# Kernel tuning notes

Hardware: AMD Instinct MI355X
Metric: run time of the kernel (lower is better)

The kernel has to match this reference:

```python
import jax, jax.numpy as jnp
import numpy as np

N = 50000
E = 800000
IN_C = 128
HID = 8
HEADS = 8
OUT_C = 16
NEG_SLOPE = 0.2


def setup_inputs() -> dict:
    key = jax.random.key(0)
    ks = jax.random.split(key, 10)
    x = jax.random.normal(ks[0], (N, IN_C), dtype=jnp.float32)
    edge_index = jax.random.randint(ks[1], (2, E), 0, N, dtype=jnp.int64)
    # layer 1: GATConv(IN_C, HID, heads=HEADS, concat=True)
    s1 = 1.0 / np.sqrt(IN_C)
    W1 = jax.random.normal(ks[2], (HEADS * HID, IN_C), dtype=jnp.float32) * s1
    att_src1 = jax.random.normal(ks[3], (HEADS, HID), dtype=jnp.float32) * 0.1
    att_dst1 = jax.random.normal(ks[4], (HEADS, HID), dtype=jnp.float32) * 0.1
    b1 = jnp.zeros((HEADS * HID,), dtype=jnp.float32)
    # layer 2: GATConv(HEADS*HID, OUT_C, heads=1, concat=False)
    s2 = 1.0 / np.sqrt(HEADS * HID)
    W2 = jax.random.normal(ks[5], (OUT_C, HEADS * HID), dtype=jnp.float32) * s2
    att_src2 = jax.random.normal(ks[6], (1, OUT_C), dtype=jnp.float32) * 0.1
    att_dst2 = jax.random.normal(ks[7], (1, OUT_C), dtype=jnp.float32) * 0.1
    b2 = jnp.zeros((OUT_C,), dtype=jnp.float32)
    return {"x": x, "edge_index": edge_index, "W1": W1, "att_src1": att_src1,
            "att_dst1": att_dst1, "b1": b1, "W2": W2, "att_src2": att_src2,
            "att_dst2": att_dst2, "b2": b2}


def _gat_conv(x, W, att_src, att_dst, bias, src, dst, concat):
    # x: [N, F_in]; W: [H*C, F_in]; att_*: [H, C]
    H, C = att_src.shape
    h = (x @ W.T).reshape(N, H, C)                       # [N, H, C]
    a_src = jnp.einsum('nhc,hc->nh', h, att_src)          # [N, H]
    a_dst = jnp.einsum('nhc,hc->nh', h, att_dst)          # [N, H]
    e = a_src[src] + a_dst[dst]                           # [Etot, H]
    e = jnp.where(e > 0, e, NEG_SLOPE * e)                # LeakyReLU(0.2)
    # segment softmax over edges grouped by destination node
    m = jax.ops.segment_max(e, dst, num_segments=N)       # [N, H]
    e = jnp.exp(e - m[dst])
    denom = jax.ops.segment_sum(e, dst, num_segments=N)   # [N, H]
    alpha = e / (denom[dst] + 1e-16)                      # [Etot, H]
    msg = alpha[:, :, None] * h[src]                      # [Etot, H, C]
    out = jax.ops.segment_sum(msg, dst, num_segments=N)   # [N, H, C]
    if concat:
        out = out.reshape(N, H * C)
    else:
        out = out.mean(axis=1)
    return out + bias


def reference(x, edge_index, W1, att_src1, att_dst1, b1, W2, att_src2, att_dst2, b2):
    # add self-loops (PyG GATConv default)
    loops = jnp.arange(N, dtype=edge_index.dtype)
    src = jnp.concatenate([edge_index[0], loops])
    dst = jnp.concatenate([edge_index[1], loops])
    h = _gat_conv(x, W1, att_src1, att_dst1, b1, src, dst, concat=True)
    h = jax.nn.elu(h)  # dropout is identity in eval mode
    return _gat_conv(h, W2, att_src2, att_dst2, b2, src, dst, concat=False)
```

## Files before the change

### kernel.cpp

```cpp
#include <hip/hip_runtime.h>
#include <hip/hip_fp16.h>
#include <math.h>

#define NN 50000
#define NE 800000
#define ETOT (NE + NN)
#define INC 128
#define F1 64
#define NH 8
#define OC 16
#define NEG 0.2f
#define BSH 7
#define NBUK 391
#define CHUNK_A 4096
#define NBLK_A ((ETOT + CHUNK_A - 1) / CHUNK_A)
#define G1TILE 64
#define NBLK_G1 ((NN + G1TILE - 1) / G1TILE)
#define XR 136

typedef _Float16 half8 __attribute__((ext_vector_type(8)));
typedef float f32x4 __attribute__((ext_vector_type(4)));

__device__ __forceinline__ float leaky(float x){ return x > 0.f ? x : NEG * x; }

__device__ __forceinline__ void getsd(const int* __restrict__ ei, int e, int& s, int& d){
    if (e < NE){ s = ei[e]; d = ei[NE + e]; }
    else { s = e - NE; d = s; }
}


__global__ __launch_bounds__(256) void zero_gbcnt(int* __restrict__ gbcnt){
    int i = blockIdx.x*256 + threadIdx.x;
    if (i < NBUK) gbcnt[i] = 0;
}

__global__ __launch_bounds__(256) void bucket_hist(const int* __restrict__ ei, int* __restrict__ gbcnt){
    __shared__ int bcnt[NBUK];
    int tid = threadIdx.x;
    for (int j = tid; j < NBUK; j += 256) bcnt[j] = 0;
    __syncthreads();
    int e0 = blockIdx.x * CHUNK_A;
    int e1 = e0 + CHUNK_A; if (e1 > ETOT) e1 = ETOT;
    for (int e = e0 + tid; e < e1; e += 256){
        int d = (e < NE) ? ei[NE + e] : e - NE;
        atomicAdd(&bcnt[d >> BSH], 1);
    }
    __syncthreads();
    for (int j = tid; j < NBUK; j += 256)
        if (bcnt[j]) atomicAdd(&gbcnt[j], bcnt[j]);
}

__global__ __launch_bounds__(512) void bucket_scan(const int* __restrict__ gbcnt,
        int* __restrict__ gboff, int* __restrict__ gbcur){
    __shared__ int s[512];
    int t = threadIdx.x;
    int v = (t < NBUK) ? gbcnt[t] : 0;
    s[t] = v; __syncthreads();
    for (int off = 1; off < 512; off <<= 1){
        int u = (t >= off) ? s[t - off] : 0;
        __syncthreads();
        s[t] += u;
        __syncthreads();
    }
    if (t < NBUK){ int ex = s[t] - v; gboff[t] = ex; gbcur[t] = ex; }
    if (t == 0) gboff[NBUK] = ETOT;
}

__global__ __launch_bounds__(256) void bucket_scatter(const int* __restrict__ ei,
        int* __restrict__ gbcur, unsigned* __restrict__ packed){
    __shared__ int bcnt[NBUK];
    int tid = threadIdx.x;
    for (int j = tid; j < NBUK; j += 256) bcnt[j] = 0;
    __syncthreads();
    int e0 = blockIdx.x * CHUNK_A;
    int e1 = e0 + CHUNK_A; if (e1 > ETOT) e1 = ETOT;
    for (int e = e0 + tid; e < e1; e += 256){
        int d = (e < NE) ? ei[NE + e] : e - NE;
        atomicAdd(&bcnt[d >> BSH], 1);
    }
    __syncthreads();
    for (int j = tid; j < NBUK; j += 256){
        int c = bcnt[j];
        bcnt[j] = c ? atomicAdd(&gbcur[j], c) : 0;
    }
    __syncthreads();
    for (int e = e0 + tid; e < e1; e += 256){
        int s, d; getsd(ei, e, s, d);
        int pos = atomicAdd(&bcnt[d >> BSH], 1);
        packed[pos] = ((unsigned)s << 16) | (unsigned)d;
    }
}

__global__ __launch_bounds__(256) void bucket_finalize(const unsigned* __restrict__ packed,
        const int* __restrict__ gboff, int* __restrict__ rowstart, int* __restrict__ esrc){
    __shared__ int ldeg[1 << BSH];
    __shared__ int lcur[1 << BSH];
    __shared__ int wtot[2];
    int b = blockIdx.x, t = threadIdx.x;
    if (t < (1 << BSH)) ldeg[t] = 0;
    __syncthreads();
    int p0 = gboff[b], p1 = gboff[b+1];
    for (int i = p0 + t; i < p1; i += 256)
        atomicAdd(&ldeg[packed[i] & ((1 << BSH) - 1)], 1);
    __syncthreads();
    if (t < (1 << BSH)){
        int v = ldeg[t];
        int lane = t & 63, w = t >> 6;
        int iv = v;
        #pragma unroll
        for (int off = 1; off < 64; off <<= 1){
            int u = __shfl_up(iv, off);
            if (lane >= off) iv += u;
        }
        lcur[t] = iv;
        if (lane == 63) wtot[w] = iv;
    }
    __syncthreads();
    if (t < (1 << BSH)){
        int v = ldeg[t];
        int w = t >> 6;
        int incl = lcur[t] + (w ? wtot[0] : 0);
        int rs = p0 + incl - v;
        int n = (b << BSH) + t;
        if (n < NN) rowstart[n] = rs;
        lcur[t] = rs;
    }
    if (b == 0 && t == 0) rowstart[NN] = ETOT;
    __syncthreads();
    for (int i = p0 + t; i < p1; i += 256){
        unsigned p = packed[i];
        int pos = atomicAdd(&lcur[p & ((1 << BSH) - 1)], 1);
        esrc[pos] = (int)(p >> 16);
    }
}

__global__ __launch_bounds__(256) void gemm1(const float* __restrict__ x, const float* __restrict__ W1,
        const float* __restrict__ att_s, const float* __restrict__ att_d,
        __half* __restrict__ h1h, float* __restrict__ a_src, float* __restrict__ a_dst){
    __shared__ _Float16 xs[64*XR];
    __shared__ _Float16 wsl[64*XR];
    int tid = threadIdx.x;
    int base = blockIdx.x * G1TILE;
    for (int i = tid; i < F1*INC; i += 256){
        int o = i >> 7, k = i & 127;
        wsl[o*XR + k] = (_Float16)W1[i];
    }
    for (int f = tid; f < 64*32; f += 256){
        int row = f >> 5, c4 = f & 31;
        int n = base + row;
        float4 v = (n < NN) ? reinterpret_cast<const float4*>(x)[n*32 + c4]
                            : make_float4(0.f,0.f,0.f,0.f);
        _Float16* p = &xs[row*XR + c4*4];
        p[0] = (_Float16)v.x; p[1] = (_Float16)v.y;
        p[2] = (_Float16)v.z; p[3] = (_Float16)v.w;
    }
    __syncthreads();
    int w = tid >> 6, lane = tid & 63;
    int mrow = lane & 15, kg = lane >> 4;
    int nodeb = w*16;
    half8 afrag[4];
    #pragma unroll
    for (int kk = 0; kk < 4; ++kk){
        const _Float16* pa = &xs[(nodeb + mrow)*XR + kk*32 + kg*4];
        *(unsigned long long*)&afrag[kk]       = *(const unsigned long long*)pa;
        *((unsigned long long*)&afrag[kk] + 1) = *(const unsigned long long*)(pa + 16);
    }
    f32x4 acc[4];
    #pragma unroll
    for (int ot = 0; ot < 4; ++ot) acc[ot] = (f32x4){0.f,0.f,0.f,0.f};
    #pragma unroll
    for (int ot = 0; ot < 4; ++ot){
        #pragma unroll
        for (int kk = 0; kk < 4; ++kk){
            const _Float16* pb = &wsl[(ot*16 + mrow)*XR + kk*32 + kg*4];
            half8 bfrag;
            *(unsigned long long*)&bfrag       = *(const unsigned long long*)pb;
            *((unsigned long long*)&bfrag + 1) = *(const unsigned long long*)(pb + 16);
            acc[ot] = __builtin_amdgcn_mfma_f32_16x16x32_f16(afrag[kk], bfrag, acc[ot], 0, 0, 0);
        }
    }
    #pragma unroll
    for (int ot = 0; ot < 4; ++ot){
        int o = ot*16 + mrow;
        float as_o = att_s[o], ad_o = att_d[o];
        #pragma unroll
        for (int r = 0; r < 4; ++r){
            float dv = acc[ot][r];
            int node = base + nodeb + kg*4 + r;
            if (node < NN) h1h[node*64 + o] = __float2half(dv);
            float ps = dv * as_o, pd = dv * ad_o;
            ps += __shfl_xor(ps, 1); ps += __shfl_xor(ps, 2); ps += __shfl_xor(ps, 4);
            pd += __shfl_xor(pd, 1); pd += __shfl_xor(pd, 2); pd += __shfl_xor(pd, 4);
            if ((lane & 7) == 0 && node < NN){
                int h = ot*2 + ((lane >> 3) & 1);
                a_src[node*8 + h] = ps;
                a_dst[node*8 + h] = pd;
            }
        }
    }
}


__global__ __launch_bounds__(256, 4) void gemm2(const float* __restrict__ out1, const float* __restrict__ W2,
        const float* __restrict__ att_s, const float* __restrict__ att_d,
        __half* __restrict__ h2h, float* __restrict__ a_src, float* __restrict__ a_dst){
    __shared__ float xs2[64*80];
    int tid = threadIdx.x;
    int base = blockIdx.x * 64;
    int w = tid >> 6, lane = tid & 63;
    int o = lane >> 2, ks = lane & 3;
    float4 wr[4];
    {
        const float4* W4 = reinterpret_cast<const float4*>(W2);
        #pragma unroll
        for (int j4 = 0; j4 < 4; ++j4)
            wr[j4] = W4[o*16 + ks*4 + j4];
    }
    float as_o = att_s[o], ad_o = att_d[o];
    {
        #pragma unroll
        for (int j = 0; j < 4; ++j){
            int f = tid + 256*j;
            int row = f >> 4, c4 = f & 15;
            int n = base + row;
            float4 v = make_float4(0.f,0.f,0.f,0.f);
            if (n < NN) v = reinterpret_cast<const float4*>(out1)[n*16 + c4];
            v.x = v.x > 0.f ? v.x : __expf(v.x) - 1.f;
            v.y = v.y > 0.f ? v.y : __expf(v.y) - 1.f;
            v.z = v.z > 0.f ? v.z : __expf(v.z) - 1.f;
            v.w = v.w > 0.f ? v.w : __expf(v.w) - 1.f;
            int sk = c4 >> 2, j4 = c4 & 3;
            *(float4*)(&xs2[row*80 + sk*20 + j4*4]) = v;
        }
    }
    __syncthreads();
    for (int r = 0; r < 16; ++r){
        int row = w*16 + r;
        const float* xb = &xs2[row*80 + ks*20];
        float acc = 0.f;
        #pragma unroll
        for (int j4 = 0; j4 < 4; ++j4){
            float4 xv = *(const float4*)(xb + j4*4);
            acc = fmaf(xv.x, wr[j4].x, acc);
            acc = fmaf(xv.y, wr[j4].y, acc);
            acc = fmaf(xv.z, wr[j4].z, acc);
            acc = fmaf(xv.w, wr[j4].w, acc);
        }
        acc += __shfl_xor(acc, 1); acc += __shfl_xor(acc, 2);
        int node = base + row;
        float ps = acc * as_o, pd = acc * ad_o;
        ps += __shfl_xor(ps, 4); ps += __shfl_xor(ps, 8);
        ps += __shfl_xor(ps, 16); ps += __shfl_xor(ps, 32);
        pd += __shfl_xor(pd, 4); pd += __shfl_xor(pd, 8);
        pd += __shfl_xor(pd, 16); pd += __shfl_xor(pd, 32);
        if (node < NN){
            if (ks == 0) h2h[node*16 + o] = __float2half(acc);
            if (lane == 0){ a_src[node] = ps; a_dst[node] = pd; }
        }
    }
}


__global__ __launch_bounds__(256) void layer1_node(const int* __restrict__ rowstart,
        const int* __restrict__ esrc, const float* __restrict__ a_src,
        const float* __restrict__ a_dst, const __half* __restrict__ h1h,
        const float* __restrict__ b1, float* __restrict__ out1){
    int wid = __builtin_amdgcn_readfirstlane((blockIdx.x*256 + threadIdx.x) >> 6);
    int lane = threadIdx.x & 63;
    if (wid >= NN) return;
    int n = wid;
    int h = lane >> 3;
    int r0 = rowstart[n], r1 = rowstart[n+1];
    float ad = a_dst[n*8 + h];
    float den0 = 0.f, acc0 = 0.f, den1 = 0.f, acc1 = 0.f;
    float den2 = 0.f, acc2 = 0.f, den3 = 0.f, acc3 = 0.f;
    float den4 = 0.f, acc4 = 0.f, den5 = 0.f, acc5 = 0.f;
    float den6 = 0.f, acc6 = 0.f, den7 = 0.f, acc7 = 0.f;
    int i = r0;
    for (; i + 7 < r1; i += 8){
        int s0 = esrc[i],   s1 = esrc[i+1], s2 = esrc[i+2], s3 = esrc[i+3];
        int s4 = esrc[i+4], s5 = esrc[i+5], s6 = esrc[i+6], s7 = esrc[i+7];
        float e0 = leaky(a_src[s0*8 + h] + ad);
        float e1 = leaky(a_src[s1*8 + h] + ad);
        float e2 = leaky(a_src[s2*8 + h] + ad);
        float e3 = leaky(a_src[s3*8 + h] + ad);
        float e4 = leaky(a_src[s4*8 + h] + ad);
        float e5 = leaky(a_src[s5*8 + h] + ad);
        float e6 = leaky(a_src[s6*8 + h] + ad);
        float e7 = leaky(a_src[s7*8 + h] + ad);
        float hv0 = __half2float(h1h[s0*64 + lane]);
        float hv1 = __half2float(h1h[s1*64 + lane]);
        float hv2 = __half2float(h1h[s2*64 + lane]);
        float hv3 = __half2float(h1h[s3*64 + lane]);
        float hv4 = __half2float(h1h[s4*64 + lane]);
        float hv5 = __half2float(h1h[s5*64 + lane]);
        float hv6 = __half2float(h1h[s6*64 + lane]);
        float hv7 = __half2float(h1h[s7*64 + lane]);
        float p0 = __expf(e0), p1 = __expf(e1), p2 = __expf(e2), p3 = __expf(e3);
        float p4 = __expf(e4), p5 = __expf(e5), p6 = __expf(e6), p7 = __expf(e7);
        den0 += p0; acc0 = fmaf(p0, hv0, acc0);
        den1 += p1; acc1 = fmaf(p1, hv1, acc1);
        den2 += p2; acc2 = fmaf(p2, hv2, acc2);
        den3 += p3; acc3 = fmaf(p3, hv3, acc3);
        den4 += p4; acc4 = fmaf(p4, hv4, acc4);
        den5 += p5; acc5 = fmaf(p5, hv5, acc5);
        den6 += p6; acc6 = fmaf(p6, hv6, acc6);
        den7 += p7; acc7 = fmaf(p7, hv7, acc7);
    }
    for (; i + 3 < r1; i += 4){
        int s0 = esrc[i], s1 = esrc[i+1], s2 = esrc[i+2], s3 = esrc[i+3];
        float e0 = leaky(a_src[s0*8 + h] + ad);
        float e1 = leaky(a_src[s1*8 + h] + ad);
        float e2 = leaky(a_src[s2*8 + h] + ad);
        float e3 = leaky(a_src[s3*8 + h] + ad);
        float hv0 = __half2float(h1h[s0*64 + lane]);
        float hv1 = __half2float(h1h[s1*64 + lane]);
        float hv2 = __half2float(h1h[s2*64 + lane]);
        float hv3 = __half2float(h1h[s3*64 + lane]);
        float p0 = __expf(e0), p1 = __expf(e1), p2 = __expf(e2), p3 = __expf(e3);
        den0 += p0; acc0 = fmaf(p0, hv0, acc0);
        den1 += p1; acc1 = fmaf(p1, hv1, acc1);
        den2 += p2; acc2 = fmaf(p2, hv2, acc2);
        den3 += p3; acc3 = fmaf(p3, hv3, acc3);
    }
    for (; i < r1; ++i){
        int s = esrc[i];
        float p = __expf(leaky(a_src[s*8 + h] + ad));
        den0 += p; acc0 = fmaf(p, __half2float(h1h[s*64 + lane]), acc0);
    }
    float den = ((den0 + den1) + (den2 + den3)) + ((den4 + den5) + (den6 + den7));
    float acc = ((acc0 + acc1) + (acc2 + acc3)) + ((acc4 + acc5) + (acc6 + acc7));
    out1[n*64 + lane] = acc/(den + 1e-16f) + b1[lane];
}

__global__ __launch_bounds__(256) void layer2_node(const int* __restrict__ rowstart,
        const int* __restrict__ esrc, const float* __restrict__ a_src,
        const float* __restrict__ a_dst, const __half* __restrict__ h2h,
        const float* __restrict__ b2, float* __restrict__ out){
    int wid = __builtin_amdgcn_readfirstlane((blockIdx.x*256 + threadIdx.x) >> 6);
    int lane = threadIdx.x & 63;
    if (wid >= NN) return;
    int n = wid;
    int slot = lane >> 4, c = lane & 15;
    int r0 = rowstart[n], r1 = rowstart[n+1];
    float ad = a_dst[n];
    float den0 = 0.f, acc0 = 0.f, den1 = 0.f, acc1 = 0.f;
    float den2 = 0.f, acc2 = 0.f, den3 = 0.f, acc3 = 0.f;
    int i = r0 + slot;
    for (; i + 12 < r1; i += 16){
        int s0 = esrc[i], s1 = esrc[i+4], s2 = esrc[i+8], s3 = esrc[i+12];
        float p0 = __expf(leaky(a_src[s0] + ad));
        float p1 = __expf(leaky(a_src[s1] + ad));
        float p2 = __expf(leaky(a_src[s2] + ad));
        float p3 = __expf(leaky(a_src[s3] + ad));
        float hv0 = __half2float(h2h[s0*16 + c]);
        float hv1 = __half2float(h2h[s1*16 + c]);
        float hv2 = __half2float(h2h[s2*16 + c]);
        float hv3 = __half2float(h2h[s3*16 + c]);
        den0 += p0; acc0 = fmaf(p0, hv0, acc0);
        den1 += p1; acc1 = fmaf(p1, hv1, acc1);
        den2 += p2; acc2 = fmaf(p2, hv2, acc2);
        den3 += p3; acc3 = fmaf(p3, hv3, acc3);
    }
    for (; i < r1; i += 4){
        int s = esrc[i];
        float p = __expf(leaky(a_src[s] + ad));
        den0 += p; acc0 = fmaf(p, __half2float(h2h[s*16 + c]), acc0);
    }
    float den = (den0 + den1) + (den2 + den3);
    float acc = (acc0 + acc1) + (acc2 + acc3);
    den += __shfl_xor(den, 16); den += __shfl_xor(den, 32);
    acc += __shfl_xor(acc, 16); acc += __shfl_xor(acc, 32);
    if (slot == 0) out[n*16 + c] = acc/(den + 1e-16f) + b2[c];
}

extern "C" void kernel_launch(void* const* d_in, const int* in_sizes, int n_in,
                              void* d_out, int out_size, void* d_ws, size_t ws_size,
                              hipStream_t stream){
    const float* x    = (const float*)d_in[0];
    const int*   ei   = (const int*)d_in[1];
    const float* W1   = (const float*)d_in[2];
    const float* as1w = (const float*)d_in[3];
    const float* ad1w = (const float*)d_in[4];
    const float* b1   = (const float*)d_in[5];
    const float* W2   = (const float*)d_in[6];
    const float* as2w = (const float*)d_in[7];
    const float* ad2w = (const float*)d_in[8];
    const float* b2   = (const float*)d_in[9];
    float* out = (float*)d_out;

    float* ws = (float*)d_ws;
    __half* h1h     = (__half*)ws;
    float* out1     = ws + (size_t)32*NN;
    int*   rowstart = (int*)(ws + (size_t)96*NN);
    int*   gbcnt    = rowstart + NN + 1;
    int*   gboff    = gbcnt + NBUK;
    int*   gbcur    = gboff + NBUK + 1;
    unsigned* packed= (unsigned*)(gbcur + NBUK);
    int*   esrc     = (int*)(packed + ETOT);
    float* a_src1 = out;
    float* a_dst1 = out + (size_t)8*NN;
    __half* h2h   = h1h;
    float* a_src2 = ws + (size_t)8*NN;
    float* a_dst2 = a_src2 + NN;

    hipLaunchKernelGGL(zero_gbcnt,      dim3(2), dim3(256), 0, stream, gbcnt);
    hipLaunchKernelGGL(bucket_hist,     dim3(NBLK_A), dim3(256), 0, stream, ei, gbcnt);
    hipLaunchKernelGGL(bucket_scan,     dim3(1), dim3(512), 0, stream, gbcnt, gboff, gbcur);
    hipLaunchKernelGGL(bucket_scatter,  dim3(NBLK_A), dim3(256), 0, stream, ei, gbcur, packed);
    hipLaunchKernelGGL(bucket_finalize, dim3(NBUK), dim3(256), 0, stream, packed, gboff, rowstart, esrc);

    hipLaunchKernelGGL(gemm1, dim3(NBLK_G1), dim3(256), 0, stream, x, W1, as1w, ad1w, h1h, a_src1, a_dst1);
    hipLaunchKernelGGL(layer1_node, dim3((NN*64 + 255)/256), dim3(256), 0, stream,
                       rowstart, esrc, a_src1, a_dst1, h1h, b1, out1);
    hipLaunchKernelGGL(gemm2, dim3((NN + 63)/64), dim3(256), 0, stream, out1, W2, as2w, ad2w, h2h, a_src2, a_dst2);
    hipLaunchKernelGGL(layer2_node, dim3((NN*64 + 255)/256), dim3(256), 0, stream,
                       rowstart, esrc, a_src2, a_dst2, h2h, b2, out);
}
```

Baseline: 123.8 us.

## Fuse edge bucket scatter with gemm1 and software-pipeline layer1 gathers

Merges the bucket_scatter and gemm1 kernels into one launch. The first NBLK_A blocks do the edge scatter and the remaining blocks do the feature GEMM, so the two independent stages run side by side and one launch is removed. Separately, the layer1 aggregation loop is restructured to issue the next batch of 8 gathers before computing on the previous batch, so memory latency overlaps with the exp/FMA work. The cost is higher register pressure in layer1_node, and the fused kernel's blocks all carry the gemm shared-memory footprint, which may limit occupancy for the scatter blocks.

```diff
diff --git a/kernel.cpp b/kernel.cpp
--- a/kernel.cpp
+++ b/kernel.cpp
@@ -66,81 +66,38 @@
     if (t == 0) gboff[NBUK] = ETOT;
 }
 
-__global__ __launch_bounds__(256) void bucket_scatter(const int* __restrict__ ei,
-        int* __restrict__ gbcur, unsigned* __restrict__ packed){
-    __shared__ int bcnt[NBUK];
-    int tid = threadIdx.x;
-    for (int j = tid; j < NBUK; j += 256) bcnt[j] = 0;
-    __syncthreads();
-    int e0 = blockIdx.x * CHUNK_A;
-    int e1 = e0 + CHUNK_A; if (e1 > ETOT) e1 = ETOT;
-    for (int e = e0 + tid; e < e1; e += 256){
-        int d = (e < NE) ? ei[NE + e] : e - NE;
-        atomicAdd(&bcnt[d >> BSH], 1);
-    }
-    __syncthreads();
-    for (int j = tid; j < NBUK; j += 256){
-        int c = bcnt[j];
-        bcnt[j] = c ? atomicAdd(&gbcur[j], c) : 0;
-    }
-    __syncthreads();
-    for (int e = e0 + tid; e < e1; e += 256){
-        int s, d; getsd(ei, e, s, d);
-        int pos = atomicAdd(&bcnt[d >> BSH], 1);
-        packed[pos] = ((unsigned)s << 16) | (unsigned)d;
-    }
-}
-
-__global__ __launch_bounds__(256) void bucket_finalize(const unsigned* __restrict__ packed,
-        const int* __restrict__ gboff, int* __restrict__ rowstart, int* __restrict__ esrc){
-    __shared__ int ldeg[1 << BSH];
-    __shared__ int lcur[1 << BSH];
-    __shared__ int wtot[2];
-    int b = blockIdx.x, t = threadIdx.x;
-    if (t < (1 << BSH)) ldeg[t] = 0;
-    __syncthreads();
-    int p0 = gboff[b], p1 = gboff[b+1];
-    for (int i = p0 + t; i < p1; i += 256)
-        atomicAdd(&ldeg[packed[i] & ((1 << BSH) - 1)], 1);
-    __syncthreads();
-    if (t < (1 << BSH)){
-        int v = ldeg[t];
-        int lane = t & 63, w = t >> 6;
-        int iv = v;
-        #pragma unroll
-        for (int off = 1; off < 64; off <<= 1){
-            int u = __shfl_up(iv, off);
-            if (lane >= off) iv += u;
-        }
-        lcur[t] = iv;
-        if (lane == 63) wtot[w] = iv;
-    }
-    __syncthreads();
-    if (t < (1 << BSH)){
-        int v = ldeg[t];
-        int w = t >> 6;
-        int incl = lcur[t] + (w ? wtot[0] : 0);
-        int rs = p0 + incl - v;
-        int n = (b << BSH) + t;
-        if (n < NN) rowstart[n] = rs;
-        lcur[t] = rs;
-    }
-    if (b == 0 && t == 0) rowstart[NN] = ETOT;
-    __syncthreads();
-    for (int i = p0 + t; i < p1; i += 256){
-        unsigned p = packed[i];
-        int pos = atomicAdd(&lcur[p & ((1 << BSH) - 1)], 1);
-        esrc[pos] = (int)(p >> 16);
-    }
-}
-
-__global__ __launch_bounds__(256) void gemm1(const float* __restrict__ x, const float* __restrict__ W1,
+__global__ __launch_bounds__(256) void scatter_gemm1(const int* __restrict__ ei,
+        int* __restrict__ gbcur, unsigned* __restrict__ packed,
+        const float* __restrict__ x, const float* __restrict__ W1,
         const float* __restrict__ att_s, const float* __restrict__ att_d,
         __half* __restrict__ h1h, float* __restrict__ a_src, float* __restrict__ a_dst){
     __shared__ _Float16 xs[64*XR];
     __shared__ _Float16 wsl[64*XR];
     int tid = threadIdx.x;
-    int base = blockIdx.x * G1TILE;
+    if (blockIdx.x < NBLK_A){
+        int* bcnt = (int*)xs;
+        for (int j = tid; j < NBUK; j += 256) bcnt[j] = 0;
+        __syncthreads();
+        int e0 = blockIdx.x * CHUNK_A;
+        int e1 = e0 + CHUNK_A; if (e1 > ETOT) e1 = ETOT;
+        for (int e = e0 + tid; e < e1; e += 256){
+            int d = (e < NE) ? ei[NE + e] : e - NE;
+            atomicAdd(&bcnt[d >> BSH], 1);
+        }
+        __syncthreads();
+        for (int j = tid; j < NBUK; j += 256){
+            int c = bcnt[j];
+            bcnt[j] = c ? atomicAdd(&gbcur[j], c) : 0;
+        }
+        __syncthreads();
+        for (int e = e0 + tid; e < e1; e += 256){
+            int s, d; getsd(ei, e, s, d);
+            int pos = atomicAdd(&bcnt[d >> BSH], 1);
+            packed[pos] = ((unsigned)s << 16) | (unsigned)d;
+        }
+        return;
+    }
+    int base = (blockIdx.x - NBLK_A) * G1TILE;
     for (int i = tid; i < F1*INC; i += 256){
         int o = i >> 7, k = i & 127;
         wsl[o*XR + k] = (_Float16)W1[i];
@@ -197,6 +154,49 @@
                 a_dst[node*8 + h] = pd;
             }
         }
+    }
+}
+
+__global__ __launch_bounds__(256) void bucket_finalize(const unsigned* __restrict__ packed,
+        const int* __restrict__ gboff, int* __restrict__ rowstart, int* __restrict__ esrc){
+    __shared__ int ldeg[1 << BSH];
+    __shared__ int lcur[1 << BSH];
+    __shared__ int wtot[2];
+    int b = blockIdx.x, t = threadIdx.x;
+    if (t < (1 << BSH)) ldeg[t] = 0;
+    __syncthreads();
+    int p0 = gboff[b], p1 = gboff[b+1];
+    for (int i = p0 + t; i < p1; i += 256)
+        atomicAdd(&ldeg[packed[i] & ((1 << BSH) - 1)], 1);
+    __syncthreads();
+    if (t < (1 << BSH)){
+        int v = ldeg[t];
+        int lane = t & 63, w = t >> 6;
+        int iv = v;
+        #pragma unroll
+        for (int off = 1; off < 64; off <<= 1){
+            int u = __shfl_up(iv, off);
+            if (lane >= off) iv += u;
+        }
+        lcur[t] = iv;
+        if (lane == 63) wtot[w] = iv;
+    }
+    __syncthreads();
+    if (t < (1 << BSH)){
+        int v = ldeg[t];
+        int w = t >> 6;
+        int incl = lcur[t] + (w ? wtot[0] : 0);
+        int rs = p0 + incl - v;
+        int n = (b << BSH) + t;
+        if (n < NN) rowstart[n] = rs;
+        lcur[t] = rs;
+    }
+    if (b == 0 && t == 0) rowstart[NN] = ETOT;
+    __syncthreads();
+    for (int i = p0 + t; i < p1; i += 256){
+        unsigned p = packed[i];
+        int pos = atomicAdd(&lcur[p & ((1 << BSH) - 1)], 1);
+        esrc[pos] = (int)(p >> 16);
     }
 }
 
@@ -277,35 +277,68 @@
     float den4 = 0.f, acc4 = 0.f, den5 = 0.f, acc5 = 0.f;
     float den6 = 0.f, acc6 = 0.f, den7 = 0.f, acc7 = 0.f;
     int i = r0;
-    for (; i + 7 < r1; i += 8){
+    int nfull = (r1 - r0) >> 3;
+    if (nfull > 0){
         int s0 = esrc[i],   s1 = esrc[i+1], s2 = esrc[i+2], s3 = esrc[i+3];
         int s4 = esrc[i+4], s5 = esrc[i+5], s6 = esrc[i+6], s7 = esrc[i+7];
-        float e0 = leaky(a_src[s0*8 + h] + ad);
-        float e1 = leaky(a_src[s1*8 + h] + ad);
-        float e2 = leaky(a_src[s2*8 + h] + ad);
-        float e3 = leaky(a_src[s3*8 + h] + ad);
-        float e4 = leaky(a_src[s4*8 + h] + ad);
-        float e5 = leaky(a_src[s5*8 + h] + ad);
-        float e6 = leaky(a_src[s6*8 + h] + ad);
-        float e7 = leaky(a_src[s7*8 + h] + ad);
-        float hv0 = __half2float(h1h[s0*64 + lane]);
-        float hv1 = __half2float(h1h[s1*64 + lane]);
-        float hv2 = __half2float(h1h[s2*64 + lane]);
-        float hv3 = __half2float(h1h[s3*64 + lane]);
-        float hv4 = __half2float(h1h[s4*64 + lane]);
-        float hv5 = __half2float(h1h[s5*64 + lane]);
-        float hv6 = __half2float(h1h[s6*64 + lane]);
-        float hv7 = __half2float(h1h[s7*64 + lane]);
-        float p0 = __expf(e0), p1 = __expf(e1), p2 = __expf(e2), p3 = __expf(e3);
-        float p4 = __expf(e4), p5 = __expf(e5), p6 = __expf(e6), p7 = __expf(e7);
-        den0 += p0; acc0 = fmaf(p0, hv0, acc0);
-        den1 += p1; acc1 = fmaf(p1, hv1, acc1);
-        den2 += p2; acc2 = fmaf(p2, hv2, acc2);
-        den3 += p3; acc3 = fmaf(p3, hv3, acc3);
-        den4 += p4; acc4 = fmaf(p4, hv4, acc4);
-        den5 += p5; acc5 = fmaf(p5, hv5, acc5);
-        den6 += p6; acc6 = fmaf(p6, hv6, acc6);
-        den7 += p7; acc7 = fmaf(p7, hv7, acc7);
+        float eA0 = a_src[s0*8 + h], eA1 = a_src[s1*8 + h];
+        float eA2 = a_src[s2*8 + h], eA3 = a_src[s3*8 + h];
+        float eA4 = a_src[s4*8 + h], eA5 = a_src[s5*8 + h];
+        float eA6 = a_src[s6*8 + h], eA7 = a_src[s7*8 + h];
+        float hA0 = __half2float(h1h[s0*64 + lane]);
+        float hA1 = __half2float(h1h[s1*64 + lane]);
+        float hA2 = __half2float(h1h[s2*64 + lane]);
+        float hA3 = __half2float(h1h[s3*64 + lane]);
+        float hA4 = __half2float(h1h[s4*64 + lane]);
+        float hA5 = __half2float(h1h[s5*64 + lane]);
+        float hA6 = __half2float(h1h[s6*64 + lane]);
+        float hA7 = __half2float(h1h[s7*64 + lane]);
+        i += 8;
+        for (int b = 1; b < nfull; ++b){
+            int t0 = esrc[i],   t1 = esrc[i+1], t2 = esrc[i+2], t3 = esrc[i+3];
+            int t4 = esrc[i+4], t5 = esrc[i+5], t6 = esrc[i+6], t7 = esrc[i+7];
+            float eB0 = a_src[t0*8 + h], eB1 = a_src[t1*8 + h];
+            float eB2 = a_src[t2*8 + h], eB3 = a_src[t3*8 + h];
+            float eB4 = a_src[t4*8 + h], eB5 = a_src[t5*8 + h];
+            float eB6 = a_src[t6*8 + h], eB7 = a_src[t7*8 + h];
+            float hB0 = __half2float(h1h[t0*64 + lane]);
+            float hB1 = __half2float(h1h[t1*64 + lane]);
+            float hB2 = __half2float(h1h[t2*64 + lane]);
+            float hB3 = __half2float(h1h[t3*64 + lane]);
+            float hB4 = __half2float(h1h[t4*64 + lane]);
+            float hB5 = __half2float(h1h[t5*64 + lane]);
+            float hB6 = __half2float(h1h[t6*64 + lane]);
+            float hB7 = __half2float(h1h[t7*64 + lane]);
+            i += 8;
+            float p0 = __expf(leaky(eA0 + ad)), p1 = __expf(leaky(eA1 + ad));
+            float p2 = __expf(leaky(eA2 + ad)), p3 = __expf(leaky(eA3 + ad));
+            float p4 = __expf(leaky(eA4 + ad)), p5 = __expf(leaky(eA5 + ad));
+            float p6 = __expf(leaky(eA6 + ad)), p7 = __expf(leaky(eA7 + ad));
+            den0 += p0; acc0 = fmaf(p0, hA0, acc0);
+            den1 += p1; acc1 = fmaf(p1, hA1, acc1);
+            den2 += p2; acc2 = fmaf(p2, hA2, acc2);
+            den3 += p3; acc3 = fmaf(p3, hA3, acc3);
+            den4 += p4; acc4 = fmaf(p4, hA4, acc4);
+            den5 += p5; acc5 = fmaf(p5, hA5, acc5);
+            den6 += p6; acc6 = fmaf(p6, hA6, acc6);
+            den7 += p7; acc7 = fmaf(p7, hA7, acc7);
+            eA0 = eB0; eA1 = eB1; eA2 = eB2; eA3 = eB3;
+            eA4 = eB4; eA5 = eB5; eA6 = eB6; eA7 = eB7;
+            hA0 = hB0; hA1 = hB1; hA2 = hB2; hA3 = hB3;
+            hA4 = hB4; hA5 = hB5; hA6 = hB6; hA7 = hB7;
+        }
+        float p0 = __expf(leaky(eA0 + ad)), p1 = __expf(leaky(eA1 + ad));
+        float p2 = __expf(leaky(eA2 + ad)), p3 = __expf(leaky(eA3 + ad));
+        float p4 = __expf(leaky(eA4 + ad)), p5 = __expf(leaky(eA5 + ad));
+        float p6 = __expf(leaky(eA6 + ad)), p7 = __expf(leaky(eA7 + ad));
+        den0 += p0; acc0 = fmaf(p0, hA0, acc0);
+        den1 += p1; acc1 = fmaf(p1, hA1, acc1);
+        den2 += p2; acc2 = fmaf(p2, hA2, acc2);
+        den3 += p3; acc3 = fmaf(p3, hA3, acc3);
+        den4 += p4; acc4 = fmaf(p4, hA4, acc4);
+        den5 += p5; acc5 = fmaf(p5, hA5, acc5);
+        den6 += p6; acc6 = fmaf(p6, hA6, acc6);
+        den7 += p7; acc7 = fmaf(p7, hA7, acc7);
     }
     for (; i + 3 < r1; i += 4){
         int s0 = esrc[i], s1 = esrc[i+1], s2 = esrc[i+2], s3 = esrc[i+3];
@@ -407,10 +440,10 @@
     hipLaunchKernelGGL(zero_gbcnt,      dim3(2), dim3(256), 0, stream, gbcnt);
     hipLaunchKernelGGL(bucket_hist,     dim3(NBLK_A), dim3(256), 0, stream, ei, gbcnt);
     hipLaunchKernelGGL(bucket_scan,     dim3(1), dim3(512), 0, stream, gbcnt, gboff, gbcur);
-    hipLaunchKernelGGL(bucket_scatter,  dim3(NBLK_A), dim3(256), 0, stream, ei, gbcur, packed);
+    hipLaunchKernelGGL(scatter_gemm1,   dim3(NBLK_A + NBLK_G1), dim3(256), 0, stream,
+                       ei, gbcur, packed, x, W1, as1w, ad1w, h1h, a_src1, a_dst1);
     hipLaunchKernelGGL(bucket_finalize, dim3(NBUK), dim3(256), 0, stream, packed, gboff, rowstart, esrc);
 
-    hipLaunchKernelGGL(gemm1, dim3(NBLK_G1), dim3(256), 0, stream, x, W1, as1w, ad1w, h1h, a_src1, a_dst1);
     hipLaunchKernelGGL(layer1_node, dim3((NN*64 + 255)/256), dim3(256), 0, stream,
                        rowstart, esrc, a_src1, a_dst1, h1h, b1, out1);
     hipLaunchKernelGGL(gemm2, dim3((NN + 63)/64), dim3(256), 0, stream, out1, W2, as2w, ad2w, h2h, a_src2, a_dst2);
```

Result: faster. 113.7 us (-8.2%).
